# Kernel optimization log

Measured on AMD Instinct MI355X. Metric: run time of the kernel, lower is better.

Reference implementation:

```python
import jax, jax.numpy as jnp
import numpy as np

N = 2048  # num_neurons == batch == input/hidden/output size (required for shape consistency)


def setup_inputs() -> dict:
    key = jax.random.key(0)
    ks = jax.random.split(key, 8)
    s = 1.0 / np.sqrt(N)
    return {
        "x": jax.random.normal(ks[0], (N, N), jnp.float32),
        "W1": jax.random.normal(ks[1], (N, N), jnp.float32) * s,
        "b1": jnp.zeros((N,), jnp.float32),
        "W2": jax.random.normal(ks[2], (N, N), jnp.float32) * s,
        "b2": jnp.zeros((N,), jnp.float32),
        "W3": jax.random.normal(ks[3], (N, N), jnp.float32) * s,
        "b3": jnp.zeros((N,), jnp.float32),
        "weights": jax.random.uniform(ks[4], (N, N), jnp.float32) * 2.0 - 1.0,
        "last_spike_time": jax.random.uniform(ks[5], (N,), jnp.float32) * 10.0,
        "membrane_potential": jnp.zeros((N,), jnp.float32),
        "n": jnp.zeros((N,), jnp.float32),
        "m": jnp.zeros((N,), jnp.float32),
        "h": jnp.zeros((N,), jnp.float32),
    }


def reference(x, W1, b1, W2, b2, W3, b3, weights, last_spike_time,
              membrane_potential, n, m, h):
    dt = 0.01
    membrane_decay = 0.5
    current_time = 10.0
    # --- Hodgkin-Huxley style dynamics (elementwise chain) ---
    v = membrane_decay * membrane_potential + jax.nn.sigmoid(x @ W1.T + b1)  # [B,N]
    spiking = v > 1.0
    v = jnp.where(spiking, 0.0, v)
    alpha_n = 0.01 * (v + 55.0) / (1.0 - jnp.exp(-(v + 55.0) / 10.0))
    beta_n = 0.125 * jnp.exp(-(v + 65.0) / 80.0)
    alpha_m = 0.1 * (v + 40.0) / (1.0 - jnp.exp(-(v + 40.0) / 10.0))
    beta_m = 4.0 * jnp.exp(-(v + 65.0) / 18.0)
    alpha_h = 0.07 * jnp.exp(-(v + 65.0) / 20.0)
    beta_h = 1.0 / (1.0 + jnp.exp(-(v + 35.0) / 10.0))
    n_new = n + dt * (alpha_n * (1.0 - n) - beta_n * n)  # [B,N]
    m_new = m + dt * (alpha_m * (1.0 - m) - beta_m * m)
    h_new = h + dt * (alpha_h * (1.0 - h) - beta_h * h)
    # --- all-pairs STDP update (vectorized form of the O(n^2) Python loop) ---
    tau_plus, tau_minus = 15.0, 25.0
    A_plus, A_minus = 0.02, 0.015
    row_spiked = jnp.any(spiking, axis=1)                 # [B] == spiking_neurons[i].any()
    pair_mask = row_spiked[:, None] | row_spiked[None, :]  # [B,B]
    ts = current_time - last_spike_time                   # [N] (B == N)
    dt_mat = ts[:, None] - ts[None, :]                    # delta_t for every pair
    dw = jnp.where(dt_mat > 0,
                   -A_minus * jnp.exp(-jnp.abs(dt_mat) / tau_minus),
                   A_plus * jnp.exp(-jnp.abs(dt_mat) / tau_plus))
    new_weights = jnp.clip(weights + jnp.where(pair_mask, dw, 0.0), -1.0, 1.0)
    # --- output MLP ---
    out = jax.nn.sigmoid(jax.nn.sigmoid(v @ W2.T + b2) @ W3.T + b3)  # [B,output]
    return out, new_weights, n_new, m_new, h_new
```

## Files before the change

kernel.cpp:

```cpp
#include <hip/hip_runtime.h>
#include <hip/hip_bf16.h>
#include <math.h>


#define NN 2048
#define BK 64
#define KHALF (NN / 2)
#define KTH (KHALF / BK)
#define NT (NN / 128)

typedef __attribute__((ext_vector_type(8))) short bf16x8;
typedef __attribute__((ext_vector_type(4))) float f32x4;
typedef __attribute__((ext_vector_type(4))) short s16x4;

__device__ __forceinline__ short f2bf(float f) {
    union { float f; unsigned u; } a; a.f = f;
    unsigned r = a.u + 0x7FFFu + ((a.u >> 16) & 1u);
    return (short)(r >> 16);
}

__device__ __forceinline__ float bf2f(short s) {
    union { unsigned u; float f; } a;
    a.u = ((unsigned)(unsigned short)s) << 16;
    return a.f;
}

__device__ __forceinline__ void gload16(const short* g, short* l) {
    __builtin_amdgcn_global_load_lds(
        (const __attribute__((address_space(1))) unsigned int*)g,
        (__attribute__((address_space(3))) unsigned int*)l, 16, 0, 0);
}

__device__ __forceinline__ float sigmoidf_(float x) {
    return 1.0f / (1.0f + expf(-x));
}

__device__ __forceinline__ void conv_item(const float* __restrict__ src,
                                          short* __restrict__ dst, int i) {
    float4 v = reinterpret_cast<const float4*>(src)[i];
    s16x4 o;
    o.x = f2bf(v.x); o.y = f2bf(v.y); o.z = f2bf(v.z); o.w = f2bf(v.w);
    reinterpret_cast<s16x4*>(dst)[i] = o;
}

__global__ void conv2_kernel(const float* __restrict__ s0, const float* __restrict__ s1,
                             short* __restrict__ d0, short* __restrict__ d1,
                             int* __restrict__ flags)
{
    int i = blockIdx.x * blockDim.x + threadIdx.x;
    if (blockIdx.y == 0) {
        conv_item(s0, d0, i);
        if (blockIdx.x < NN / 256)
            flags[blockIdx.x * blockDim.x + threadIdx.x] = 0;
    } else {
        conv_item(s1, d1, i);
    }
}

__device__ __forceinline__ void gemm_body(
    const short* __restrict__ A, const short* __restrict__ B,
    short* __restrict__ P, short (*As)[128 * BK], short (*Bs)[128 * BK])
{
    const int tid  = threadIdx.x;
    const int lane = tid & 63;
    const int wid  = tid >> 6;
    const int row0 = blockIdx.y * 128;
    const int col0 = blockIdx.x * 128;
    const int kbase = blockIdx.z * KHALF;
    const int wm   = (wid >> 2) * 64;
    const int wn   = (wid & 3) * 32;
    const int lrow = lane & 15;
    const int lk16 = (lane >> 4) << 3;

    f32x4 acc[4][2] = {};

    auto stage = [&](int buf, int k0) {
#pragma unroll
        for (int s = 0; s < 2; ++s) {
            int c = tid + s * 512;
            int r = c >> 3;
            int ksrc = ((c & 7) ^ (r & 7)) << 3;
            gload16(A + (size_t)(row0 + r) * NN + k0 + ksrc, &As[buf][c * 8]);
            gload16(B + (size_t)(col0 + r) * NN + k0 + ksrc, &Bs[buf][c * 8]);
        }
    };

    auto compute = [&](int buf) {
        bf16x8 af[4][2], bfv[2][2];
#pragma unroll
        for (int i = 0; i < 4; ++i) {
            const int row = wm + i * 16 + lrow;
#pragma unroll
            for (int kk = 0; kk < 2; ++kk) {
                const int ke = (lk16 + kk * 32) ^ ((row & 7) << 3);
                af[i][kk] = *reinterpret_cast<const bf16x8*>(&As[buf][row * BK + ke]);
            }
        }
#pragma unroll
        for (int j = 0; j < 2; ++j) {
            const int row = wn + j * 16 + lrow;
#pragma unroll
            for (int kk = 0; kk < 2; ++kk) {
                const int ke = (lk16 + kk * 32) ^ ((row & 7) << 3);
                bfv[j][kk] = *reinterpret_cast<const bf16x8*>(&Bs[buf][row * BK + ke]);
            }
        }
#pragma unroll
        for (int kk = 0; kk < 2; ++kk)
#pragma unroll
            for (int i = 0; i < 4; ++i)
#pragma unroll
                for (int j = 0; j < 2; ++j)
                    acc[i][j] = __builtin_amdgcn_mfma_f32_16x16x32_bf16(
                        af[i][kk], bfv[j][kk], acc[i][j], 0, 0, 0);
    };

    stage(0, kbase);
    __syncthreads();
    int cur = 0;
    for (int t = 0; t < KTH - 1; ++t) {
        stage(cur ^ 1, kbase + (t + 1) * BK);
        compute(cur);
        __syncthreads();
        cur ^= 1;
    }
    compute(cur);

    short* outp = P + (size_t)blockIdx.z * NN * NN;
#pragma unroll
    for (int i = 0; i < 4; ++i) {
#pragma unroll
        for (int j = 0; j < 2; ++j) {
            const int gcol = col0 + wn + j * 16 + lrow;
#pragma unroll
            for (int r = 0; r < 4; ++r) {
                const int grow = row0 + wm + i * 16 + ((lane >> 4) << 2) + r;
                outp[(size_t)grow * NN + gcol] = f2bf(acc[i][j][r]);
            }
        }
    }
}

__global__ __launch_bounds__(512) void gemm_partial(
    const short* __restrict__ A, const short* __restrict__ B,
    short* __restrict__ P)
{
    __shared__ short As[2][128 * BK] __attribute__((aligned(16)));
    __shared__ short Bs[2][128 * BK] __attribute__((aligned(16)));
    gemm_body(A, B, P, As, Bs);
}

__global__ __launch_bounds__(512) void gemm_stdp(
    const short* __restrict__ A, const short* __restrict__ B,
    short* __restrict__ P,
    const float* __restrict__ w, const float* __restrict__ lst,
    const int* __restrict__ flags, float* __restrict__ outw)
{
    __shared__ short As[2][128 * BK] __attribute__((aligned(16)));
    __shared__ short Bs[2][128 * BK] __attribute__((aligned(16)));
    if (blockIdx.z == 2) {
        const int bflat = blockIdx.y * gridDim.x + blockIdx.x;
#pragma unroll
        for (int u = 0; u < 8; ++u) {
            int idx = bflat * 4096 + u * 512 + threadIdx.x;
            int i  = idx >> 9;
            int j4 = (idx & 511) << 2;
            float4 wv = reinterpret_cast<const float4*>(w)[idx];
            float o[4] = {wv.x, wv.y, wv.z, wv.w};
            const int   rsi = flags[i];
            const float tsi = 10.0f - lst[i];
#pragma unroll
            for (int t = 0; t < 4; ++t) {
                int j = j4 + t;
                if (rsi | flags[j]) {
                    float dtm = tsi - (10.0f - lst[j]);
                    float dw = (dtm > 0.0f) ? (-0.015f * expf(-fabsf(dtm) / 25.0f))
                                            : ( 0.02f  * expf(-fabsf(dtm) / 15.0f));
                    o[t] += dw;
                }
                o[t] = fminf(1.0f, fmaxf(-1.0f, o[t]));
            }
            reinterpret_cast<float4*>(outw)[idx] = make_float4(o[0], o[1], o[2], o[3]);
        }
        return;
    }
    gemm_body(A, B, P, As, Bs);
}

__global__ void comb1_mix(
    const short* __restrict__ p0, const short* __restrict__ p1,
    const float* __restrict__ bias,
    const float* __restrict__ mp,
    const float* __restrict__ n_in, const float* __restrict__ m_in,
    const float* __restrict__ h_in,
    short* __restrict__ out_v,
    float* __restrict__ out_n, float* __restrict__ out_m,
    float* __restrict__ out_h,
    int* __restrict__ flags,
    const float* __restrict__ convsrc, short* __restrict__ convdst)
{
    int idx = blockIdx.x * blockDim.x + threadIdx.x;
    if (blockIdx.y == 1) { conv_item(convsrc, convdst, idx); return; }
    int row = idx >> 9;
    int g   = idx & 511;
    s16x4 a = reinterpret_cast<const s16x4*>(p0)[idx];
    s16x4 b = reinterpret_cast<const s16x4*>(p1)[idx];
    float4 bi = reinterpret_cast<const float4*>(bias)[g];
    float pre[4] = { bf2f(a.x) + bf2f(b.x) + bi.x,
                     bf2f(a.y) + bf2f(b.y) + bi.y,
                     bf2f(a.z) + bf2f(b.z) + bi.z,
                     bf2f(a.w) + bf2f(b.w) + bi.w };
    float4 mp4 = reinterpret_cast<const float4*>(mp)[g];
    float4 n4  = reinterpret_cast<const float4*>(n_in)[g];
    float4 m4  = reinterpret_cast<const float4*>(m_in)[g];
    float4 h4  = reinterpret_cast<const float4*>(h_in)[g];
    float mpv[4] = {mp4.x, mp4.y, mp4.z, mp4.w};
    float nv[4]  = {n4.x, n4.y, n4.z, n4.w};
    float mv[4]  = {m4.x, m4.y, m4.z, m4.w};
    float hv[4]  = {h4.x, h4.y, h4.z, h4.w};
    s16x4 vb;
    float on[4], om[4], oh[4];
#pragma unroll
    for (int t = 0; t < 4; ++t) {
        float v = 0.5f * mpv[t] + sigmoidf_(pre[t]);
        if (v > 1.0f) { flags[row] = 1; v = 0.0f; }
        vb[t] = f2bf(v);
        float an = 0.01f * (v + 55.0f) / (1.0f - expf(-(v + 55.0f) / 10.0f));
        float bn = 0.125f * expf(-(v + 65.0f) / 80.0f);
        float am = 0.1f  * (v + 40.0f) / (1.0f - expf(-(v + 40.0f) / 10.0f));
        float bm = 4.0f  * expf(-(v + 65.0f) / 18.0f);
        float ah = 0.07f * expf(-(v + 65.0f) / 20.0f);
        float bh = 1.0f  / (1.0f + expf(-(v + 35.0f) / 10.0f));
        on[t] = nv[t] + 0.01f * (an * (1.0f - nv[t]) - bn * nv[t]);
        om[t] = mv[t] + 0.01f * (am * (1.0f - mv[t]) - bm * mv[t]);
        oh[t] = hv[t] + 0.01f * (ah * (1.0f - hv[t]) - bh * hv[t]);
    }
    reinterpret_cast<s16x4*>(out_v)[idx] = vb;
    reinterpret_cast<float4*>(out_n)[idx] = make_float4(on[0], on[1], on[2], on[3]);
    reinterpret_cast<float4*>(out_m)[idx] = make_float4(om[0], om[1], om[2], om[3]);
    reinterpret_cast<float4*>(out_h)[idx] = make_float4(oh[0], oh[1], oh[2], oh[3]);
}

__global__ void comb2_mix(
    const short* __restrict__ p0, const short* __restrict__ p1,
    const float* __restrict__ bias,
    short* __restrict__ out_bf,
    const float* __restrict__ convsrc, short* __restrict__ convdst)
{
    int idx = blockIdx.x * blockDim.x + threadIdx.x;
    if (blockIdx.y == 1) { conv_item(convsrc, convdst, idx); return; }
    int g = idx & 511;
    s16x4 a = reinterpret_cast<const s16x4*>(p0)[idx];
    s16x4 b = reinterpret_cast<const s16x4*>(p1)[idx];
    float4 bi = reinterpret_cast<const float4*>(bias)[g];
    s16x4 o;
    o.x = f2bf(sigmoidf_(bf2f(a.x) + bf2f(b.x) + bi.x));
    o.y = f2bf(sigmoidf_(bf2f(a.y) + bf2f(b.y) + bi.y));
    o.z = f2bf(sigmoidf_(bf2f(a.z) + bf2f(b.z) + bi.z));
    o.w = f2bf(sigmoidf_(bf2f(a.w) + bf2f(b.w) + bi.w));
    reinterpret_cast<s16x4*>(out_bf)[idx] = o;
}

__global__ void combine3(
    const short* __restrict__ p0, const short* __restrict__ p1,
    const float* __restrict__ bias, float* __restrict__ out_f)
{
    int idx = blockIdx.x * blockDim.x + threadIdx.x;
    int g = idx & 511;
    s16x4 a = reinterpret_cast<const s16x4*>(p0)[idx];
    s16x4 b = reinterpret_cast<const s16x4*>(p1)[idx];
    float4 bi = reinterpret_cast<const float4*>(bias)[g];
    reinterpret_cast<float4*>(out_f)[idx] = make_float4(
        sigmoidf_(bf2f(a.x) + bf2f(b.x) + bi.x),
        sigmoidf_(bf2f(a.y) + bf2f(b.y) + bi.y),
        sigmoidf_(bf2f(a.z) + bf2f(b.z) + bi.z),
        sigmoidf_(bf2f(a.w) + bf2f(b.w) + bi.w));
}

extern "C" void kernel_launch(void* const* d_in, const int* in_sizes, int n_in,
                              void* d_out, int out_size, void* d_ws, size_t ws_size,
                              hipStream_t stream)
{
    const float* x   = (const float*)d_in[0];
    const float* W1  = (const float*)d_in[1];
    const float* b1  = (const float*)d_in[2];
    const float* W2  = (const float*)d_in[3];
    const float* b2  = (const float*)d_in[4];
    const float* W3  = (const float*)d_in[5];
    const float* b3  = (const float*)d_in[6];
    const float* wts = (const float*)d_in[7];
    const float* lst = (const float*)d_in[8];
    const float* mp  = (const float*)d_in[9];
    const float* nin = (const float*)d_in[10];
    const float* min_ = (const float*)d_in[11];
    const float* hin = (const float*)d_in[12];

    const size_t NSQ = (size_t)NN * NN;
    float* out    = (float*)d_out;
    float* out_w  = out + NSQ;
    float* out_n  = out + 2 * NSQ;
    float* out_m  = out + 3 * NSQ;
    float* out_h  = out + 4 * NSQ;

    short* R1 = (short*)d_ws;
    short* R2 = R1 + NSQ;
    short* R3 = R2 + NSQ;
    short* R4 = R3 + NSQ;
    short* P  = R4 + NSQ;
    int* flags = (int*)(P + 2 * NSQ);

    const int convBlocks = (int)(NSQ / 4 / 256);

    conv2_kernel<<<dim3(convBlocks, 2), 256, 0, stream>>>(x, W1, R1, R2, flags);
    gemm_partial<<<dim3(NT, NT, 2), 512, 0, stream>>>(R1, R2, P);
    comb1_mix<<<dim3(convBlocks, 2), 256, 0, stream>>>(
        P, P + NSQ, b1, mp, nin, min_, hin,
        R3, out_n, out_m, out_h, flags, W2, R4);
    gemm_stdp<<<dim3(NT, NT, 3), 512, 0, stream>>>(R3, R4, P, wts, lst, flags, out_w);
    comb2_mix<<<dim3(convBlocks, 2), 256, 0, stream>>>(
        P, P + NSQ, b2, R2, W3, R1);
    gemm_partial<<<dim3(NT, NT, 2), 512, 0, stream>>>(R2, R1, P);
    combine3<<<convBlocks, 256, 0, stream>>>(P, P + NSQ, b3, out);
}
```

Baseline: 123.7 us.

## Split K across warp pairs with 64x64 warp tiles and LDS reduction

Each group of four warps now owns a 64x64 output sub-tile, and the two warp groups split each BK=64 slice in half along K. This raises MFMA work per LDS fragment load, since each warp loads 4+4 fragments for 16 MFMAs instead of 8+4 for 16. The two halves' accumulators are summed through shared memory at the end, which adds an extra sync and an LDS round trip. Launch bounds now request 4 blocks per SM, which limits registers per thread while the accumulator array has doubled, so spills are possible.

```diff
diff --git a/kernel.cpp b/kernel.cpp
--- a/kernel.cpp
+++ b/kernel.cpp
@@ -64,15 +64,17 @@
     const int tid  = threadIdx.x;
     const int lane = tid & 63;
     const int wid  = tid >> 6;
+    const int tw   = wid & 3;
+    const int kh   = wid >> 2;
     const int row0 = blockIdx.y * 128;
     const int col0 = blockIdx.x * 128;
     const int kbase = blockIdx.z * KHALF;
-    const int wm   = (wid >> 2) * 64;
-    const int wn   = (wid & 3) * 32;
+    const int wm   = (tw >> 1) * 64;
+    const int wn   = (tw & 1) * 64;
     const int lrow = lane & 15;
-    const int lk16 = (lane >> 4) << 3;
-
-    f32x4 acc[4][2] = {};
+    const int lkk  = ((lane >> 4) << 3) + kh * 32;
+
+    f32x4 acc[4][4] = {};
 
     auto stage = [&](int buf, int k0) {
 #pragma unroll
@@ -86,33 +88,25 @@
     };
 
     auto compute = [&](int buf) {
-        bf16x8 af[4][2], bfv[2][2];
+        bf16x8 af[4], bfv[4];
 #pragma unroll
         for (int i = 0; i < 4; ++i) {
             const int row = wm + i * 16 + lrow;
-#pragma unroll
-            for (int kk = 0; kk < 2; ++kk) {
-                const int ke = (lk16 + kk * 32) ^ ((row & 7) << 3);
-                af[i][kk] = *reinterpret_cast<const bf16x8*>(&As[buf][row * BK + ke]);
-            }
-        }
-#pragma unroll
-        for (int j = 0; j < 2; ++j) {
+            const int ke  = lkk ^ ((row & 7) << 3);
+            af[i] = *reinterpret_cast<const bf16x8*>(&As[buf][row * BK + ke]);
+        }
+#pragma unroll
+        for (int j = 0; j < 4; ++j) {
             const int row = wn + j * 16 + lrow;
-#pragma unroll
-            for (int kk = 0; kk < 2; ++kk) {
-                const int ke = (lk16 + kk * 32) ^ ((row & 7) << 3);
-                bfv[j][kk] = *reinterpret_cast<const bf16x8*>(&Bs[buf][row * BK + ke]);
-            }
-        }
-#pragma unroll
-        for (int kk = 0; kk < 2; ++kk)
-#pragma unroll
-            for (int i = 0; i < 4; ++i)
-#pragma unroll
-                for (int j = 0; j < 2; ++j)
-                    acc[i][j] = __builtin_amdgcn_mfma_f32_16x16x32_bf16(
-                        af[i][kk], bfv[j][kk], acc[i][j], 0, 0, 0);
+            const int ke  = lkk ^ ((row & 7) << 3);
+            bfv[j] = *reinterpret_cast<const bf16x8*>(&Bs[buf][row * BK + ke]);
+        }
+#pragma unroll
+        for (int i = 0; i < 4; ++i)
+#pragma unroll
+            for (int j = 0; j < 4; ++j)
+                acc[i][j] = __builtin_amdgcn_mfma_f32_16x16x32_bf16(
+                    af[i], bfv[j], acc[i][j], 0, 0, 0);
     };
 
     stage(0, kbase);
@@ -126,22 +120,40 @@
     }
     compute(cur);
 
-    short* outp = P + (size_t)blockIdx.z * NN * NN;
-#pragma unroll
-    for (int i = 0; i < 4; ++i) {
-#pragma unroll
-        for (int j = 0; j < 2; ++j) {
-            const int gcol = col0 + wn + j * 16 + lrow;
-#pragma unroll
-            for (int r = 0; r < 4; ++r) {
-                const int grow = row0 + wm + i * 16 + ((lane >> 4) << 2) + r;
-                outp[(size_t)grow * NN + gcol] = f2bf(acc[i][j][r]);
+    __syncthreads();
+    if (kh == 1) {
+        float* dst = (tw < 2) ? (float*)As : (float*)Bs;
+        dst += (tw & 1) * 4096;
+#pragma unroll
+        for (int f = 0; f < 16; ++f)
+            reinterpret_cast<f32x4*>(dst)[f * 64 + lane] = acc[f >> 2][f & 3];
+    }
+    __syncthreads();
+    if (kh == 0) {
+        const float* src = (tw < 2) ? (const float*)As : (const float*)Bs;
+        src += (tw & 1) * 4096;
+#pragma unroll
+        for (int f = 0; f < 16; ++f) {
+            f32x4 o = reinterpret_cast<const f32x4*>(src)[f * 64 + lane];
+            acc[f >> 2][f & 3] += o;
+        }
+        short* outp = P + (size_t)blockIdx.z * NN * NN;
+#pragma unroll
+        for (int i = 0; i < 4; ++i) {
+#pragma unroll
+            for (int j = 0; j < 4; ++j) {
+                const int gcol = col0 + wn + j * 16 + lrow;
+#pragma unroll
+                for (int r = 0; r < 4; ++r) {
+                    const int grow = row0 + wm + i * 16 + ((lane >> 4) << 2) + r;
+                    outp[(size_t)grow * NN + gcol] = f2bf(acc[i][j][r]);
+                }
             }
         }
     }
 }
 
-__global__ __launch_bounds__(512) void gemm_partial(
+__global__ __launch_bounds__(512, 4) void gemm_partial(
     const short* __restrict__ A, const short* __restrict__ B,
     short* __restrict__ P)
 {
@@ -150,7 +162,7 @@
     gemm_body(A, B, P, As, Bs);
 }
 
-__global__ __launch_bounds__(512) void gemm_stdp(
+__global__ __launch_bounds__(512, 4) void gemm_stdp(
     const short* __restrict__ A, const short* __restrict__ B,
     short* __restrict__ P,
     const float* __restrict__ w, const float* __restrict__ lst,
```

Result: slower. 129.5 us (+4.7%).
